# Performance work log

Measured on AMD Instinct MI355X. Metric: run time of the kernel, lower is better.

The kernel has to match this reference:

```python
import jax, jax.numpy as jnp
import numpy as np

N, E, F, H, G, C = 50000, 800000, 128, 64, 512, 10
RATIO = 0.5  # forward arg `ratio` baked as constant


def seg_mean(msgs, idx, n):
    s = jax.ops.segment_sum(msgs, idx, num_segments=n)
    cnt = jax.ops.segment_sum(jnp.ones(idx.shape[0], msgs.dtype), idx, num_segments=n)
    return s / jnp.maximum(cnt, 1.0)[:, None]


def sage(x, src, dst, Wl, bl, Wr, ew=None):
    # PyG SAGEConv: lin_l(mean_{j->i} msg_j) + lin_r(x_i); weighted variant scales messages
    m = x[src] if ew is None else x[src] * ew[:, None]
    agg = seg_mean(m, dst, x.shape[0])
    return agg @ Wl + bl + x @ Wr


def topk_mask(scores, seg, num_graphs, ratio):
    # per-graph (segment) top-k edge selection: keep ceil(ratio*edges_in_graph) highest scores
    e = scores.shape[0]
    counts = jax.ops.segment_sum(jnp.ones(e, jnp.float32), seg, num_segments=num_graphs)
    order = jnp.lexsort((-scores, seg))  # sort by segment, then score descending
    seg_sorted = seg[order]
    starts = jnp.concatenate([jnp.zeros(1, jnp.float32), jnp.cumsum(counts)[:-1]])
    rank = jnp.arange(e, dtype=jnp.float32) - starts[seg_sorted]
    k = jnp.ceil(ratio * counts)
    sel = (rank < k[seg_sorted]).astype(scores.dtype)
    return jnp.zeros(e, scores.dtype).at[order].set(sel)


def setup_inputs():
    key = jax.random.key(0)
    ks = jax.random.split(key, 16)
    w = lambda k, shape, fan: (jax.random.normal(k, shape, jnp.float32) / np.sqrt(fan))
    return {
        'x': jax.random.normal(ks[0], (N, F), jnp.float32),
        'edge_index': jax.random.randint(ks[1], (2, E), 0, N, jnp.int32),
        'batch': jnp.sort(jax.random.randint(ks[2], (N,), 0, G, jnp.int32)),
        'W1l': w(ks[3], (F, H), F), 'b1l': jnp.zeros(H, jnp.float32), 'W1r': w(ks[4], (F, H), F),
        'W2l': w(ks[5], (H, H), H), 'b2l': jnp.zeros(H, jnp.float32), 'W2r': w(ks[6], (H, H), H),
        'W3l': w(ks[7], (H, H), H), 'b3l': jnp.zeros(H, jnp.float32), 'W3r': w(ks[8], (H, H), H),
        'Wlin1': w(ks[9], (H, H), H), 'blin1': jnp.zeros(H, jnp.float32),
        'Wlin2': w(ks[10], (H, C), H), 'blin2': jnp.zeros(C, jnp.float32),
    }


def reference(x, edge_index, batch, W1l, b1l, W1r, W2l, b2l, W2r, W3l, b3l, W3r, Wlin1, blin1, Wlin2, blin2):
    src, dst = edge_index[0], edge_index[1]
    h = jax.nn.relu(sage(x, src, dst, W1l, b1l, W1r))
    edge_scores = jnp.sum(h[src] * h[dst], axis=-1)  # [E]
    seg = batch[src]  # graph id per edge (sections)
    sampled = topk_mask(edge_scores, seg, G, RATIO)
    ew = edge_scores * sampled
    h = jax.nn.relu(sage(h, src, dst, W2l, b2l, W2r, ew))
    h = jax.nn.relu(sage(h, src, dst, W3l, b3l, W3r, ew))
    pooled = seg_mean(h, batch, G)  # global_mean_pool
    z = jax.nn.relu(pooled @ Wlin1 + blin1)
    z = z @ Wlin2 + blin2  # dropout inactive in eval
    return jax.nn.log_softmax(z, axis=-1), sampled
```

## Files before the change

kernel.cpp:

```cpp
#include <hip/hip_runtime.h>
#include <hip/hip_bf16.h>
#include <math.h>

static constexpr int N = 50000;
static constexpr int E = 800000;
static constexpr int F = 128;
static constexpr int H = 64;
static constexpr int G = 512;
static constexpr int C = 10;
static constexpr int CAP = 256;
static constexpr int NFB = (E / 4 + 255) / 256;
static constexpr int GB1 = N / 16;
static constexpr int GB2 = (N + 31) / 32;
static constexpr int SB = E / 256;

static inline int cdiv(long a, int b) { return (int)((a + b - 1) / b); }

__device__ __forceinline__ float uinv_score(unsigned u) {
  return (u & 0x80000000u) ? __uint_as_float(u & 0x7fffffffu) : __uint_as_float(~u);
}

__device__ __forceinline__ int2 pack_slot(int s, int d, int g, int e) {
  unsigned a = (unsigned)s | ((unsigned)(d & 0x7FFF) << 17);
  unsigned b = ((unsigned)d >> 15) | ((unsigned)g << 2) | ((unsigned)e << 11);
  return make_int2((int)a, (int)b);
}
__device__ __forceinline__ int slot_src(int2 p) { return p.x & 0x1FFFF; }
__device__ __forceinline__ int slot_dst(int2 p) {
  return (int)(((unsigned)p.x >> 17) | (((unsigned)p.y & 3u) << 15));
}
__device__ __forceinline__ int slot_g(int2 p) { return (int)(((unsigned)p.y >> 2) & 0x1FFu); }
__device__ __forceinline__ int slot_eid(int2 p) { return (int)((unsigned)p.y >> 11); }

__global__ void k_deg_goff(const int* __restrict__ dst, const int* __restrict__ batch,
                           int* __restrict__ deg, int* __restrict__ goff,
                           unsigned short* __restrict__ rank16) {
  int tid = threadIdx.x;
  for (int i = blockIdx.x * 256 + tid; i < N; i += gridDim.x * 256) {
    int b = batch[i];
    if (i == 0) {
      for (int g = 0; g <= b; ++g) goff[g] = 0;
    } else {
      int p = batch[i - 1];
      for (int g = p + 1; g <= b; ++g) goff[g] = i;
    }
    if (i == N - 1) {
      for (int g = b + 1; g <= G; ++g) goff[g] = N;
    }
  }
  const int4* d4 = (const int4*)dst;
  for (int i = blockIdx.x * 256 + tid; i < E / 4; i += gridDim.x * 256) {
    int4 v = d4[i];
    ushort4 rk;
    rk.x = (unsigned short)atomicAdd(&deg[v.x], 1);
    rk.y = (unsigned short)atomicAdd(&deg[v.y], 1);
    rk.z = (unsigned short)atomicAdd(&deg[v.z], 1);
    rk.w = (unsigned short)atomicAdd(&deg[v.w], 1);
    *(ushort4*)(rank16 + (size_t)i * 4) = rk;
  }
}

__global__ void k_scan_a(const int* __restrict__ cnt, int* __restrict__ off,
                         int* __restrict__ bsum, int n) {
  __shared__ int wsum[16];
  int tid = threadIdx.x, lane = tid & 63, wv = tid >> 6;
  int idx = blockIdx.x * 4096 + tid * 4;
  int v0 = (idx + 0 < n) ? cnt[idx + 0] : 0;
  int v1 = (idx + 1 < n) ? cnt[idx + 1] : 0;
  int v2 = (idx + 2 < n) ? cnt[idx + 2] : 0;
  int v3 = (idx + 3 < n) ? cnt[idx + 3] : 0;
  int local = v0 + v1 + v2 + v3;
  int inc = local;
  for (int d = 1; d < 64; d <<= 1) {
    int t = __shfl_up(inc, d);
    if (lane >= d) inc += t;
  }
  if (lane == 63) wsum[wv] = inc;
  __syncthreads();
  if (tid < 16) {
    int t = wsum[tid];
    for (int d = 1; d < 16; d <<= 1) {
      int u = __shfl_up(t, d);
      if (tid >= d) t += u;
    }
    wsum[tid] = t;
  }
  __syncthreads();
  int woff = (wv > 0) ? wsum[wv - 1] : 0;
  int excl = woff + inc - local;
  if (idx + 0 < n) off[idx + 0] = excl;
  if (idx + 1 < n) off[idx + 1] = excl + v0;
  if (idx + 2 < n) off[idx + 2] = excl + v0 + v1;
  if (idx + 3 < n) off[idx + 3] = excl + v0 + v1 + v2;
  if (tid == 0) bsum[blockIdx.x] = wsum[15];
}

__global__ void k_scan_c(int* __restrict__ off, const int* __restrict__ bsum, int n, int nb) {
  __shared__ int spre[34];
  int tid = threadIdx.x;
  if (tid < 32) {
    int v = (tid < nb) ? bsum[tid] : 0;
    int inc = v;
    for (int d = 1; d < 32; d <<= 1) {
      int t = __shfl_up(inc, d);
      if (tid >= d) inc += t;
    }
    spre[tid] = inc - v;
  }
  __syncthreads();
  int i = blockIdx.x * 256 + tid;
  if (i < n) {
    off[i] = off[i] + spre[i >> 12];
  } else if (i == n) {
    off[n] = spre[nb];
  }
}

__global__ void k_fill_gemm(const int* __restrict__ src, const int* __restrict__ dst,
                            const unsigned short* __restrict__ rank16,
                            const int* __restrict__ batch, const int* __restrict__ off,
                            int2* __restrict__ csrp, int* __restrict__ einv,
                            const float* __restrict__ x, const float* __restrict__ Wl,
                            const float* __restrict__ Wr, const float* __restrict__ bl,
                            float* __restrict__ y, float* __restrict__ r) {
  __shared__ float sx[16][F];
  int lane = threadIdx.x, ty = threadIdx.y;
  int tid = ty * 64 + lane;
  int bq = blockIdx.x / 5, br = blockIdx.x - bq * 5;
  if (br == 0) {
    int i = bq * 256 + tid;
    if (i < E / 4) {
      int4 dv = ((const int4*)dst)[i];
      int4 sv = ((const int4*)src)[i];
      ushort4 rv = *(const ushort4*)(rank16 + (size_t)i * 4);
      int dd[4] = {dv.x, dv.y, dv.z, dv.w};
      int ss[4] = {sv.x, sv.y, sv.z, sv.w};
      int rr[4] = {rv.x, rv.y, rv.z, rv.w};
      int e0 = i * 4;
      int slots[4];
#pragma unroll
      for (int j = 0; j < 4; ++j) {
        int g = batch[ss[j]];
        int slot = off[dd[j]] + rr[j];
        csrp[slot] = pack_slot(ss[j], dd[j], g, e0 + j);
        slots[j] = slot;
      }
      *(int4*)(einv + e0) = make_int4(slots[0], slots[1], slots[2], slots[3]);
    }
    return;
  }
  int gid = bq * 4 + (br - 1);
  if (gid >= GB1) return;
  int row0 = gid * 16;
  const float4* gsrc = (const float4*)(x + (size_t)row0 * F);
  float4* sdst = (float4*)(&sx[0][0]);
#pragma unroll
  for (int i = tid; i < 16 * F / 4; i += 256) sdst[i] = gsrc[i];
  __syncthreads();
  float al[4], ar[4];
  float bias = bl[lane];
#pragma unroll
  for (int j = 0; j < 4; ++j) { al[j] = 0.f; ar[j] = bias; }
#pragma unroll 4
  for (int f = 0; f < F; ++f) {
    float wl = Wl[f * H + lane];
    float wr = Wr[f * H + lane];
#pragma unroll
    for (int j = 0; j < 4; ++j) {
      float xv = sx[ty * 4 + j][f];
      al[j] += xv * wl;
      ar[j] += xv * wr;
    }
  }
#pragma unroll
  for (int j = 0; j < 4; ++j) {
    int row = row0 + ty * 4 + j;
    y[(size_t)row * H + lane] = al[j];
    r[(size_t)row * H + lane] = ar[j];
  }
}

template <int K>
__global__ void k_gemm2h(const float* __restrict__ in, const float* __restrict__ Wl,
                         const float* __restrict__ Wr, const float* __restrict__ b,
                         __hip_bfloat16* __restrict__ y, float* __restrict__ r) {
  __shared__ float sx[16][K];
  int lane = threadIdx.x, ty = threadIdx.y;
  int tid = ty * 64 + lane;
  int row0 = blockIdx.x * 16;
  const float4* gsrc = (const float4*)(in + (size_t)row0 * K);
  float4* sdst = (float4*)(&sx[0][0]);
#pragma unroll
  for (int i = tid; i < 16 * K / 4; i += 256) sdst[i] = gsrc[i];
  __syncthreads();
  float al[4], ar[4];
  float bias = b[lane];
#pragma unroll
  for (int j = 0; j < 4; ++j) { al[j] = 0.f; ar[j] = bias; }
#pragma unroll 4
  for (int f = 0; f < K; ++f) {
    float wl = Wl[f * H + lane];
    float wr = Wr[f * H + lane];
#pragma unroll
    for (int j = 0; j < 4; ++j) {
      float xv = sx[ty * 4 + j][f];
      al[j] += xv * wl;
      ar[j] += xv * wr;
    }
  }
#pragma unroll
  for (int j = 0; j < 4; ++j) {
    int row = row0 + ty * 4 + j;
    y[(size_t)row * H + lane] = __float2bfloat16(al[j]);
    r[(size_t)row * H + lane] = ar[j];
  }
}

__global__ void k_agg1(const float* __restrict__ y, const float* __restrict__ r,
                       const int2* __restrict__ csrp, const int* __restrict__ off,
                       float* __restrict__ out) {
  int node = blockIdx.x * 8 + threadIdx.y;
  int lane = threadIdx.x;
  int q = lane >> 3, c = lane & 7;
  int s0 = off[node], s1 = off[node + 1];
  float4 a0 = make_float4(0.f, 0.f, 0.f, 0.f);
  float4 a1 = make_float4(0.f, 0.f, 0.f, 0.f);
  int i = s0 + q;
  for (; i + 8 < s1; i += 16) {
    int se0 = slot_src(csrp[i]);
    int se1 = slot_src(csrp[i + 8]);
    const float4* p0 = (const float4*)(y + (size_t)se0 * H);
    const float4* p1 = (const float4*)(y + (size_t)se1 * H);
    float4 u0 = p0[c], v0 = p0[c + 8];
    float4 u1 = p1[c], v1 = p1[c + 8];
    a0.x += u0.x + u1.x; a0.y += u0.y + u1.y; a0.z += u0.z + u1.z; a0.w += u0.w + u1.w;
    a1.x += v0.x + v1.x; a1.y += v0.y + v1.y; a1.z += v0.z + v1.z; a1.w += v0.w + v1.w;
  }
  for (; i < s1; i += 8) {
    int se = slot_src(csrp[i]);
    const float4* p = (const float4*)(y + (size_t)se * H);
    float4 u = p[c], v = p[c + 8];
    a0.x += u.x; a0.y += u.y; a0.z += u.z; a0.w += u.w;
    a1.x += v.x; a1.y += v.y; a1.z += v.z; a1.w += v.w;
  }
#pragma unroll
  for (int d = 8; d < 64; d <<= 1) {
    a0.x += __shfl_xor(a0.x, d); a0.y += __shfl_xor(a0.y, d);
    a0.z += __shfl_xor(a0.z, d); a0.w += __shfl_xor(a0.w, d);
    a1.x += __shfl_xor(a1.x, d); a1.y += __shfl_xor(a1.y, d);
    a1.z += __shfl_xor(a1.z, d); a1.w += __shfl_xor(a1.w, d);
  }
  if (q == 0) {
    float inv = 1.f / fmaxf((float)(s1 - s0), 1.f);
    const float4* rp = (const float4*)(r + (size_t)node * H);
    float4 r0 = rp[c], r1 = rp[c + 8];
    float4 o0, o1;
    o0.x = fmaxf(a0.x * inv + r0.x, 0.f); o0.y = fmaxf(a0.y * inv + r0.y, 0.f);
    o0.z = fmaxf(a0.z * inv + r0.z, 0.f); o0.w = fmaxf(a0.w * inv + r0.w, 0.f);
    o1.x = fmaxf(a1.x * inv + r1.x, 0.f); o1.y = fmaxf(a1.y * inv + r1.y, 0.f);
    o1.z = fmaxf(a1.z * inv + r1.z, 0.f); o1.w = fmaxf(a1.w * inv + r1.w, 0.f);
    float4* op = (float4*)(out + (size_t)node * H);
    op[c] = o0; op[c + 8] = o1;
  }
}

__global__ void k_agg_w(const __hip_bfloat16* __restrict__ y, const float* __restrict__ r,
                        const int2* __restrict__ csr2, const int* __restrict__ cnt2,
                        const int* __restrict__ off, float* __restrict__ out) {
  int node = blockIdx.x * 8 + threadIdx.y;
  int lane = threadIdx.x;
  int q = lane >> 3, c = lane & 7;
  int b0 = off[node], cn = cnt2[node];
  float a[8] = {0.f, 0.f, 0.f, 0.f, 0.f, 0.f, 0.f, 0.f};
  for (int j = q; j < cn; j += 8) {
    int2 sw = csr2[b0 + j];
    float w = __int_as_float(sw.y);
    uint4 pk = ((const uint4*)((const unsigned short*)y + (size_t)sw.x * H))[c];
    a[0] += w * __uint_as_float(pk.x << 16); a[1] += w * __uint_as_float(pk.x & 0xffff0000u);
    a[2] += w * __uint_as_float(pk.y << 16); a[3] += w * __uint_as_float(pk.y & 0xffff0000u);
    a[4] += w * __uint_as_float(pk.z << 16); a[5] += w * __uint_as_float(pk.z & 0xffff0000u);
    a[6] += w * __uint_as_float(pk.w << 16); a[7] += w * __uint_as_float(pk.w & 0xffff0000u);
  }
#pragma unroll
  for (int d = 8; d < 64; d <<= 1) {
#pragma unroll
    for (int j = 0; j < 8; ++j) a[j] += __shfl_xor(a[j], d);
  }
  if (q == 0) {
    int degn = off[node + 1] - off[node];
    float inv = 1.f / fmaxf((float)degn, 1.f);
    const float4* rp = (const float4*)(r + (size_t)node * H);
    float4 r0 = rp[2 * c], r1 = rp[2 * c + 1];
    float4 o0, o1;
    o0.x = fmaxf(a[0] * inv + r0.x, 0.f); o0.y = fmaxf(a[1] * inv + r0.y, 0.f);
    o0.z = fmaxf(a[2] * inv + r0.z, 0.f); o0.w = fmaxf(a[3] * inv + r0.w, 0.f);
    o1.x = fmaxf(a[4] * inv + r1.x, 0.f); o1.y = fmaxf(a[5] * inv + r1.y, 0.f);
    o1.z = fmaxf(a[6] * inv + r1.z, 0.f); o1.w = fmaxf(a[7] * inv + r1.w, 0.f);
    float4* op = (float4*)(out + (size_t)node * H);
    op[2 * c] = o0; op[2 * c + 1] = o1;
  }
}

__global__ void k_score_g2h(const float* __restrict__ h1, const int2* __restrict__ csrp,
                            unsigned* __restrict__ scoreu_csr,
                            unsigned short* __restrict__ seg_csr, int* __restrict__ hist,
                            const float* __restrict__ Wl, const float* __restrict__ Wr,
                            const float* __restrict__ bl,
                            __hip_bfloat16* __restrict__ y, float* __restrict__ r) {
  __shared__ float sx[32][H];
  int lane = threadIdx.x, ty = threadIdx.y;
  int q3 = blockIdx.x / 3, r3 = blockIdx.x - q3 * 3;
  if (r3 == 0 && q3 < GB2) {
    int tid = ty * 64 + lane;
    int row0 = q3 * 32;
    {
      int row = row0 + (tid >> 4);
      if (row < N)
        ((float4*)(&sx[0][0]))[tid] = ((const float4*)h1)[(size_t)row * (H / 4) + (tid & 15)];
    }
    __syncthreads();
    float al[4], ar[4];
    float bias = bl[lane];
#pragma unroll
    for (int j = 0; j < 4; ++j) { al[j] = 0.f; ar[j] = bias; }
#pragma unroll 4
    for (int f = 0; f < H; ++f) {
      float wl = Wl[f * H + lane];
      float wr = Wr[f * H + lane];
#pragma unroll
      for (int j = 0; j < 4; ++j) {
        float xv = sx[ty * 4 + j][f];
        al[j] += xv * wl;
        ar[j] += xv * wr;
      }
    }
#pragma unroll
    for (int j = 0; j < 4; ++j) {
      int row = row0 + ty * 4 + j;
      if (row < N) {
        y[(size_t)row * H + lane] = __float2bfloat16(al[j]);
        r[(size_t)row * H + lane] = ar[j];
      }
    }
  } else {
    int sid = blockIdx.x - (q3 + (r3 > 0 ? 1 : 0));
    int q = lane >> 4, c = lane & 15;
    int s = (sid * 8 + ty) * 32 + q * 8;
    int2 se[8];
#pragma unroll
    for (int j = 0; j < 8; ++j) se[j] = csrp[s + j];
    float4 xr[8], yr[8];
#pragma unroll
    for (int j = 0; j < 8; ++j)
      xr[j] = ((const float4*)(h1 + (size_t)slot_src(se[j]) * H))[c];
#pragma unroll
    for (int j = 0; j < 8; ++j)
      yr[j] = ((const float4*)(h1 + (size_t)slot_dst(se[j]) * H))[c];
    float p[8];
#pragma unroll
    for (int j = 0; j < 8; ++j)
      p[j] = yr[j].x * xr[j].x + yr[j].y * xr[j].y + yr[j].z * xr[j].z + yr[j].w * xr[j].w;
#pragma unroll
    for (int d = 1; d < 16; d <<= 1) {
#pragma unroll
      for (int j = 0; j < 8; ++j) p[j] += __shfl_xor(p[j], d);
    }
    if (c == 0) {
#pragma unroll
      for (int j = 0; j < 8; ++j) {
        int g = slot_g(se[j]);
        unsigned u = __float_as_uint(p[j]);
        u = (u & 0x80000000u) ? ~u : (u | 0x80000000u);
        scoreu_csr[s + j] = u;
        seg_csr[s + j] = (unsigned short)g;
        atomicAdd(&hist[g * 256 + (int)(u >> 24)], 1);
      }
    }
  }
}

__global__ void k_hist(const unsigned* __restrict__ scoreu, const unsigned short* __restrict__ seg,
                       const unsigned* __restrict__ prefix, int* __restrict__ hist, int pass) {
  int e = (blockIdx.x * 256 + threadIdx.x) * 4;
  if (e >= E) return;
  uint4 u4 = *(const uint4*)(scoreu + e);
  ushort4 s4 = *(const ushort4*)(seg + e);
  unsigned uu[4] = {u4.x, u4.y, u4.z, u4.w};
  int gg[4] = {(int)s4.x, (int)s4.y, (int)s4.z, (int)s4.w};
  int predshift = 32 - 8 * pass;
  int bshift = 24 - 8 * pass;
#pragma unroll
  for (int j = 0; j < 4; ++j) {
    unsigned u = uu[j];
    int g = gg[j];
    if ((u >> predshift) == (prefix[g] >> predshift))
      atomicAdd(&hist[g * 256 + (int)((u >> bshift) & 0xFFu)], 1);
  }
}

__global__ void k_scan(int* __restrict__ hist, unsigned* __restrict__ prefix,
                       int* __restrict__ krem, int pass) {
  int g = blockIdx.x;
  int lane = threadIdx.x;
  int4* row = (int4*)(hist + (size_t)g * 256);
  int4 v = row[lane];
  int vj[4] = {v.x, v.y, v.z, v.w};
  int s = v.x + v.y + v.z + v.w;
  int inc = s;
  for (int d = 1; d < 64; d <<= 1) {
    int t = __shfl_up(inc, d);
    if (lane >= d) inc += t;
  }
  int T = __shfl(inc, 63);
  int k = (pass == 0) ? ((T + 1) >> 1) : krem[g];
  int excl = inc - s;
  int pre[4] = {excl, excl + vj[0], excl + vj[0] + vj[1], excl + vj[0] + vj[1] + vj[2]};
  int bsel_l = -1, newk_l = 0;
  if (k > 0) {
    for (int j = 3; j >= 0; --j) {
      int suf = T - pre[j];
      if (suf >= k) { bsel_l = 4 * lane + j; newk_l = k - (suf - vj[j]); break; }
    }
  }
  unsigned long long mask = __ballot(bsel_l >= 0);
  int bsel = 255, newk = 0;
  if (k > 0 && mask) {
    int hi = 63 - __builtin_clzll(mask);
    bsel = __shfl(bsel_l, hi);
    newk = __shfl(newk_l, hi);
  }
  if (lane == 0) {
    unsigned base = (pass == 0) ? 0u : prefix[g];
    prefix[g] = base | ((unsigned)bsel << (24 - 8 * pass));
    krem[g] = newk;
  }
  row[lane] = make_int4(0, 0, 0, 0);
}

__global__ void k_select(const unsigned* __restrict__ scoreu_csr,
                         const unsigned short* __restrict__ seg_csr,
                         const unsigned* __restrict__ thresh,
                         int* __restrict__ eqcnt, int* __restrict__ eqlist,
                         unsigned char* __restrict__ sel_csr, float* __restrict__ ew_csr) {
  int s = (blockIdx.x * 256 + threadIdx.x) * 4;
  if (s >= E) return;
  uint4 u4 = *(const uint4*)(scoreu_csr + s);
  ushort4 g4 = *(const ushort4*)(seg_csr + s);
  unsigned uu[4] = {u4.x, u4.y, u4.z, u4.w};
  int gg[4] = {(int)g4.x, (int)g4.y, (int)g4.z, (int)g4.w};
  float ew[4];
  unsigned char sl[4];
#pragma unroll
  for (int j = 0; j < 4; ++j) {
    unsigned u = uu[j];
    int g = gg[j];
    unsigned t = thresh[g];
    unsigned um = u & 0xffffff00u;
    float sel = 0.f;
    if (um > t) sel = 1.f;
    else if (um == t) {
      int slot = atomicAdd(&eqcnt[g], 1);
      if (slot < CAP) eqlist[g * CAP + slot] = s + j;
    }
    sl[j] = (unsigned char)sel;
    ew[j] = uinv_score(u) * sel;
  }
  *(uchar4*)(sel_csr + s) = make_uchar4(sl[0], sl[1], sl[2], sl[3]);
  *(float4*)(ew_csr + s) = make_float4(ew[0], ew[1], ew[2], ew[3]);
}

__global__ void k_resolve(const int* __restrict__ krem, const int* __restrict__ eqcnt,
                          const int* __restrict__ eqlist, const int2* __restrict__ csrp,
                          const unsigned* __restrict__ scoreu_csr,
                          unsigned char* __restrict__ sel_csr, float* __restrict__ ew_csr) {
  int g = blockIdx.x * 256 + threadIdx.x;
  if (g >= G) return;
  int c = eqcnt[g]; if (c > CAP) c = CAP;
  int r = krem[g];  if (r > c) r = c;
  const int* lst = eqlist + g * CAP;
  unsigned last_u = 0u; int last_e = -1; bool first = true;
  for (int i = 0; i < r; ++i) {
    unsigned bu = 0u; int be = -1, bs = -1;
    for (int j = 0; j < c; ++j) {
      int slot = lst[j];
      unsigned u = scoreu_csr[slot];
      int eid = slot_eid(csrp[slot]);
      bool after = first || (u < last_u) || (u == last_u && eid > last_e);
      if (after && (bs < 0 || u > bu || (u == bu && eid < be))) { bu = u; be = eid; bs = slot; }
    }
    if (bs < 0) break;
    sel_csr[bs] = 1;
    ew_csr[bs] = uinv_score(bu);
    last_u = bu; last_e = be; first = false;
  }
}

__global__ void k_samp_comp(const unsigned char* __restrict__ sel,
                            const int2* __restrict__ csrp, const float* __restrict__ ewc,
                            const int* __restrict__ off, int2* __restrict__ csr2,
                            int* __restrict__ cnt2,
                            const int* __restrict__ einv, float* __restrict__ sampled) {
  int lane = threadIdx.x, ty = threadIdx.y;
  if (blockIdx.x < N / 8) {
    int node = blockIdx.x * 8 + ty;
    int s0 = off[node], s1 = off[node + 1];
    unsigned long long lt = ((unsigned long long)1 << lane) - 1;
    int cum = 0;
    for (int i0 = s0; i0 < s1; i0 += 64) {
      int i = i0 + lane;
      bool f = (i < s1) && sel[i];
      unsigned long long m = __ballot(f);
      if (f) {
        int rank = __popcll(m & lt);
        csr2[s0 + cum + rank] = make_int2(slot_src(csrp[i]), __float_as_int(ewc[i]));
      }
      cum += __popcll(m);
    }
    if (lane == 0) cnt2[node] = cum;
  } else {
    int tid = ty * 64 + lane;
    int e = ((blockIdx.x - N / 8) * 512 + tid) * 4;
    if (e >= E) return;
    int4 iv = *(const int4*)(einv + e);
    float4 o;
    o.x = (float)sel[iv.x];
    o.y = (float)sel[iv.y];
    o.z = (float)sel[iv.z];
    o.w = (float)sel[iv.w];
    *(float4*)(sampled + e) = o;
  }
}

__global__ void k_poolhead(const float* __restrict__ h3, const int* __restrict__ goff,
                           const float* __restrict__ W1, const float* __restrict__ b1,
                           const float* __restrict__ W2, const float* __restrict__ b2,
                           float* __restrict__ outp) {
  int g = blockIdx.x;
  int tid = threadIdx.x;
  int h = tid & 63, j = tid >> 6;
  int s0 = goff[g], s1 = goff[g + 1];
  float a = 0.f;
  for (int n = s0 + j; n < s1; n += 8) a += h3[(size_t)n * H + h];
  __shared__ float sp[8][H];
  __shared__ float p[H], z1[H], z2[C];
  __shared__ float lse;
  sp[j][h] = a;
  __syncthreads();
  if (j == 0) {
    float s = sp[0][h] + sp[1][h] + sp[2][h] + sp[3][h]
            + sp[4][h] + sp[5][h] + sp[6][h] + sp[7][h];
    float inv = 1.f / fmaxf((float)(s1 - s0), 1.f);
    p[h] = s * inv;
  }
  __syncthreads();
  if (j == 0) {
    float acc = b1[h];
#pragma unroll 8
    for (int f = 0; f < H; ++f) acc += p[f] * W1[f * H + h];
    z1[h] = fmaxf(acc, 0.f);
  }
  __syncthreads();
  if (tid < C) {
    float a2 = b2[tid];
#pragma unroll 8
    for (int f = 0; f < H; ++f) a2 += z1[f] * W2[f * C + tid];
    z2[tid] = a2;
  }
  __syncthreads();
  if (tid == 0) {
    float m = z2[0];
    for (int c = 1; c < C; ++c) m = fmaxf(m, z2[c]);
    float s = 0.f;
    for (int c = 0; c < C; ++c) s += expf(z2[c] - m);
    lse = m + logf(s);
  }
  __syncthreads();
  if (tid < C) outp[(size_t)g * C + tid] = z2[tid] - lse;
}

extern "C" void kernel_launch(void* const* d_in, const int* in_sizes, int n_in,
                              void* d_out, int out_size, void* d_ws, size_t ws_size,
                              hipStream_t stream) {
  const float* x     = (const float*)d_in[0];
  const int*   ei    = (const int*)d_in[1];
  const int*   batch = (const int*)d_in[2];
  const float* W1l   = (const float*)d_in[3];
  const float* b1l   = (const float*)d_in[4];
  const float* W1r   = (const float*)d_in[5];
  const float* W2l   = (const float*)d_in[6];
  const float* b2l   = (const float*)d_in[7];
  const float* W2r   = (const float*)d_in[8];
  const float* W3l   = (const float*)d_in[9];
  const float* b3l   = (const float*)d_in[10];
  const float* W3r   = (const float*)d_in[11];
  const float* Wlin1 = (const float*)d_in[12];
  const float* blin1 = (const float*)d_in[13];
  const float* Wlin2 = (const float*)d_in[14];
  const float* blin2 = (const float*)d_in[15];

  const int* srcv = ei;
  const int* dstv = ei + E;

  float* out_ls   = (float*)d_out;
  float* out_samp = out_ls + G * C;

  char* w = (char*)d_ws;
  auto carve = [&](size_t bytes) { void* p = (void*)w; w += (bytes + 255) & ~(size_t)255; return p; };
  char* zbase   = w;
  int*      deg     = (int*)carve((size_t)N * 4);
  int*      eqcnt   = (int*)carve((size_t)G * 4);
  int*      hist    = (int*)carve((size_t)G * 256 * 4);
  size_t    zbytes  = (size_t)(w - zbase);
  float*    h1      = (float*)carve((size_t)N * H * 4);
  float*    h2      = (float*)carve((size_t)N * H * 4);
  float*    h3      = (float*)carve((size_t)N * H * 4);
  float*    yb      = (float*)carve((size_t)N * H * 4);
  float*    rb      = (float*)carve((size_t)N * H * 4);
  __hip_bfloat16* ybh = (__hip_bfloat16*)carve((size_t)N * H * 2);
  unsigned* scoreu_csr = (unsigned*)carve((size_t)E * 4);
  unsigned short* seg_csr = (unsigned short*)carve((size_t)E * 2);
  float*    ew_csr     = (float*)carve((size_t)E * 4);
  unsigned char* sel_csr = (unsigned char*)carve((size_t)E);
  int2*     csrp    = (int2*)carve((size_t)E * 8);
  int*      einv    = (int*)carve((size_t)E * 4);
  unsigned short* rank16 = (unsigned short*)carve((size_t)E * 2);
  int*      off     = (int*)carve((size_t)(N + 1) * 4);
  int*      cnt2    = (int*)carve((size_t)N * 4);
  int*      goff    = (int*)carve((size_t)(G + 1) * 4);
  unsigned* prefix  = (unsigned*)carve((size_t)G * 4);
  int*      krem    = (int*)carve((size_t)G * 4);
  int*      eqlist  = (int*)carve((size_t)G * CAP * 4);
  int*      bsum    = (int*)carve((size_t)16 * 4);
  int2*     csr2    = (int2*)carve((size_t)E * 8);

  hipMemsetAsync(zbase, 0, zbytes, stream);

  k_deg_goff<<<256, 256, 0, stream>>>(dstv, batch, deg, goff, rank16);
  int nb = cdiv(N, 4096);
  k_scan_a<<<nb, 1024, 0, stream>>>(deg, off, bsum, N);
  k_scan_c<<<cdiv(N + 1, 256), 256, 0, stream>>>(off, bsum, N, nb);

  k_fill_gemm<<<5 * NFB, dim3(64, 4), 0, stream>>>(srcv, dstv, rank16, batch, off,
                                                   csrp, einv,
                                                   x, W1l, W1r, b1l, yb, rb);

  k_agg1<<<N / 8, dim3(64, 8), 0, stream>>>(yb, rb, csrp, off, h1);

  k_score_g2h<<<SB + GB2, dim3(64, 8), 0, stream>>>(h1, csrp, scoreu_csr, seg_csr, hist,
                                                    W2l, W2r, b2l, ybh, rb);
  k_scan<<<G, 64, 0, stream>>>(hist, prefix, krem, 0);
  for (int p = 1; p <= 2; ++p) {
    k_hist<<<cdiv(E / 4, 256), 256, 0, stream>>>(scoreu_csr, seg_csr, prefix, hist, p);
    k_scan<<<G, 64, 0, stream>>>(hist, prefix, krem, p);
  }
  k_select<<<cdiv(E / 4, 256), 256, 0, stream>>>(scoreu_csr, seg_csr, prefix,
                                                 eqcnt, eqlist, sel_csr, ew_csr);
  k_resolve<<<cdiv(G, 256), 256, 0, stream>>>(krem, eqcnt, eqlist, csrp, scoreu_csr,
                                              sel_csr, ew_csr);

  k_samp_comp<<<N / 8 + cdiv(E / 4, 512), dim3(64, 8), 0, stream>>>(
      sel_csr, csrp, ew_csr, off, csr2, cnt2, einv, out_samp);

  k_agg_w<<<N / 8, dim3(64, 8), 0, stream>>>(ybh, rb, csr2, cnt2, off, h2);

  k_gemm2h<H><<<N / 16, dim3(64, 4), 0, stream>>>(h2, W3l, W3r, b3l, ybh, rb);
  k_agg_w<<<N / 8, dim3(64, 8), 0, stream>>>(ybh, rb, csr2, cnt2, off, h3);

  k_poolhead<<<G, 512, 0, stream>>>(h3, goff, Wlin1, blin1, Wlin2, blin2, out_ls);
}
```

Measured before the change: 405.4 us.

## Fuse layer-2 aggregation with layer-3 GEMM and drop edge-weight buffer

Merges the weighted layer-2 aggregation with the layer-3 dual GEMM, so h2 stays in shared memory instead of being written to and reread from global memory, and one kernel launch goes away. The separate ew_csr array is removed: select and resolve now write only the selection flag, and the compaction kernel recomputes the weight from the score bits. The degree/graph-offset kernel also gets twice as many blocks. The fused GEMM runs per node with 64 threads reading W3 from global memory and no row tiling, so weight reuse may be lower than in the old 16-row GEMM. Separate ybh2/rb2 buffers are added so the kernel does not overwrite inputs that other blocks are still reading.

New measurement: 424.4 us. 4.7% more time.

```diff
diff --git a/kernel.cpp b/kernel.cpp
--- a/kernel.cpp
+++ b/kernel.cpp
@@ -180,42 +180,6 @@
   }
 }
 
-template <int K>
-__global__ void k_gemm2h(const float* __restrict__ in, const float* __restrict__ Wl,
-                         const float* __restrict__ Wr, const float* __restrict__ b,
-                         __hip_bfloat16* __restrict__ y, float* __restrict__ r) {
-  __shared__ float sx[16][K];
-  int lane = threadIdx.x, ty = threadIdx.y;
-  int tid = ty * 64 + lane;
-  int row0 = blockIdx.x * 16;
-  const float4* gsrc = (const float4*)(in + (size_t)row0 * K);
-  float4* sdst = (float4*)(&sx[0][0]);
-#pragma unroll
-  for (int i = tid; i < 16 * K / 4; i += 256) sdst[i] = gsrc[i];
-  __syncthreads();
-  float al[4], ar[4];
-  float bias = b[lane];
-#pragma unroll
-  for (int j = 0; j < 4; ++j) { al[j] = 0.f; ar[j] = bias; }
-#pragma unroll 4
-  for (int f = 0; f < K; ++f) {
-    float wl = Wl[f * H + lane];
-    float wr = Wr[f * H + lane];
-#pragma unroll
-    for (int j = 0; j < 4; ++j) {
-      float xv = sx[ty * 4 + j][f];
-      al[j] += xv * wl;
-      ar[j] += xv * wr;
-    }
-  }
-#pragma unroll
-  for (int j = 0; j < 4; ++j) {
-    int row = row0 + ty * 4 + j;
-    y[(size_t)row * H + lane] = __float2bfloat16(al[j]);
-    r[(size_t)row * H + lane] = ar[j];
-  }
-}
-
 __global__ void k_agg1(const float* __restrict__ y, const float* __restrict__ r,
                        const int2* __restrict__ csrp, const int* __restrict__ off,
                        float* __restrict__ out) {
@@ -264,6 +228,59 @@
   }
 }
 
+__global__ void k_agg_w_p3(const __hip_bfloat16* __restrict__ y, const float* __restrict__ r,
+                           const int2* __restrict__ csr2, const int* __restrict__ cnt2,
+                           const int* __restrict__ off, const unsigned* __restrict__ scoreu,
+                           const float* __restrict__ W3l, const float* __restrict__ W3r,
+                           const float* __restrict__ b3,
+                           __hip_bfloat16* __restrict__ ybh2, float* __restrict__ rb2) {
+  __shared__ float sh[8][H];
+  int node = blockIdx.x * 8 + threadIdx.y;
+  int lane = threadIdx.x;
+  int ty = threadIdx.y;
+  int q = lane >> 3, c = lane & 7;
+  int b0 = off[node], cn = cnt2[node];
+  float a[8] = {0.f, 0.f, 0.f, 0.f, 0.f, 0.f, 0.f, 0.f};
+  for (int j = q; j < cn; j += 8) {
+    int2 sw = csr2[b0 + j];
+    float w = __int_as_float(sw.y);
+    uint4 pk = ((const uint4*)((const unsigned short*)y + (size_t)sw.x * H))[c];
+    a[0] += w * __uint_as_float(pk.x << 16); a[1] += w * __uint_as_float(pk.x & 0xffff0000u);
+    a[2] += w * __uint_as_float(pk.y << 16); a[3] += w * __uint_as_float(pk.y & 0xffff0000u);
+    a[4] += w * __uint_as_float(pk.z << 16); a[5] += w * __uint_as_float(pk.z & 0xffff0000u);
+    a[6] += w * __uint_as_float(pk.w << 16); a[7] += w * __uint_as_float(pk.w & 0xffff0000u);
+  }
+#pragma unroll
+  for (int d = 8; d < 64; d <<= 1) {
+#pragma unroll
+    for (int j = 0; j < 8; ++j) a[j] += __shfl_xor(a[j], d);
+  }
+  if (q == 0) {
+    int degn = off[node + 1] - off[node];
+    float inv = 1.f / fmaxf((float)degn, 1.f);
+    const float4* rp = (const float4*)(r + (size_t)node * H);
+    float4 r0 = rp[2 * c], r1 = rp[2 * c + 1];
+    sh[ty][8 * c + 0] = fmaxf(a[0] * inv + r0.x, 0.f);
+    sh[ty][8 * c + 1] = fmaxf(a[1] * inv + r0.y, 0.f);
+    sh[ty][8 * c + 2] = fmaxf(a[2] * inv + r0.z, 0.f);
+    sh[ty][8 * c + 3] = fmaxf(a[3] * inv + r0.w, 0.f);
+    sh[ty][8 * c + 4] = fmaxf(a[4] * inv + r1.x, 0.f);
+    sh[ty][8 * c + 5] = fmaxf(a[5] * inv + r1.y, 0.f);
+    sh[ty][8 * c + 6] = fmaxf(a[6] * inv + r1.z, 0.f);
+    sh[ty][8 * c + 7] = fmaxf(a[7] * inv + r1.w, 0.f);
+  }
+  __syncthreads();
+  float al = 0.f, ar = b3[lane];
+#pragma unroll 4
+  for (int f = 0; f < H; ++f) {
+    float v = sh[ty][f];
+    al += v * W3l[f * H + lane];
+    ar += v * W3r[f * H + lane];
+  }
+  ybh2[(size_t)node * H + lane] = __float2bfloat16(al);
+  rb2[(size_t)node * H + lane] = ar;
+}
+
 __global__ void k_agg_w(const __hip_bfloat16* __restrict__ y, const float* __restrict__ r,
                         const int2* __restrict__ csr2, const int* __restrict__ cnt2,
                         const int* __restrict__ off, float* __restrict__ out) {
@@ -441,14 +458,13 @@
                          const unsigned short* __restrict__ seg_csr,
                          const unsigned* __restrict__ thresh,
                          int* __restrict__ eqcnt, int* __restrict__ eqlist,
-                         unsigned char* __restrict__ sel_csr, float* __restrict__ ew_csr) {
+                         unsigned char* __restrict__ sel_csr) {
   int s = (blockIdx.x * 256 + threadIdx.x) * 4;
   if (s >= E) return;
   uint4 u4 = *(const uint4*)(scoreu_csr + s);
   ushort4 g4 = *(const ushort4*)(seg_csr + s);
   unsigned uu[4] = {u4.x, u4.y, u4.z, u4.w};
   int gg[4] = {(int)g4.x, (int)g4.y, (int)g4.z, (int)g4.w};
-  float ew[4];
   unsigned char sl[4];
 #pragma unroll
   for (int j = 0; j < 4; ++j) {
@@ -456,23 +472,21 @@
     int g = gg[j];
     unsigned t = thresh[g];
     unsigned um = u & 0xffffff00u;
-    float sel = 0.f;
-    if (um > t) sel = 1.f;
+    unsigned char sel = 0;
+    if (um > t) sel = 1;
     else if (um == t) {
       int slot = atomicAdd(&eqcnt[g], 1);
       if (slot < CAP) eqlist[g * CAP + slot] = s + j;
     }
-    sl[j] = (unsigned char)sel;
-    ew[j] = uinv_score(u) * sel;
+    sl[j] = sel;
   }
   *(uchar4*)(sel_csr + s) = make_uchar4(sl[0], sl[1], sl[2], sl[3]);
-  *(float4*)(ew_csr + s) = make_float4(ew[0], ew[1], ew[2], ew[3]);
 }
 
 __global__ void k_resolve(const int* __restrict__ krem, const int* __restrict__ eqcnt,
                           const int* __restrict__ eqlist, const int2* __restrict__ csrp,
                           const unsigned* __restrict__ scoreu_csr,
-                          unsigned char* __restrict__ sel_csr, float* __restrict__ ew_csr) {
+                          unsigned char* __restrict__ sel_csr) {
   int g = blockIdx.x * 256 + threadIdx.x;
   if (g >= G) return;
   int c = eqcnt[g]; if (c > CAP) c = CAP;
@@ -490,13 +504,13 @@
     }
     if (bs < 0) break;
     sel_csr[bs] = 1;
-    ew_csr[bs] = uinv_score(bu);
     last_u = bu; last_e = be; first = false;
   }
 }
 
 __global__ void k_samp_comp(const unsigned char* __restrict__ sel,
-                            const int2* __restrict__ csrp, const float* __restrict__ ewc,
+                            const int2* __restrict__ csrp,
+                            const unsigned* __restrict__ scoreu,
                             const int* __restrict__ off, int2* __restrict__ csr2,
                             int* __restrict__ cnt2,
                             const int* __restrict__ einv, float* __restrict__ sampled) {
@@ -512,7 +526,8 @@
       unsigned long long m = __ballot(f);
       if (f) {
         int rank = __popcll(m & lt);
-        csr2[s0 + cum + rank] = make_int2(slot_src(csrp[i]), __float_as_int(ewc[i]));
+        float w = uinv_score(scoreu[i]);
+        csr2[s0 + cum + rank] = make_int2(slot_src(csrp[i]), __float_as_int(w));
       }
       cum += __popcll(m);
     }
@@ -612,14 +627,14 @@
   int*      hist    = (int*)carve((size_t)G * 256 * 4);
   size_t    zbytes  = (size_t)(w - zbase);
   float*    h1      = (float*)carve((size_t)N * H * 4);
-  float*    h2      = (float*)carve((size_t)N * H * 4);
   float*    h3      = (float*)carve((size_t)N * H * 4);
   float*    yb      = (float*)carve((size_t)N * H * 4);
   float*    rb      = (float*)carve((size_t)N * H * 4);
-  __hip_bfloat16* ybh = (__hip_bfloat16*)carve((size_t)N * H * 2);
+  float*    rb2     = (float*)carve((size_t)N * H * 4);
+  __hip_bfloat16* ybh  = (__hip_bfloat16*)carve((size_t)N * H * 2);
+  __hip_bfloat16* ybh2 = (__hip_bfloat16*)carve((size_t)N * H * 2);
   unsigned* scoreu_csr = (unsigned*)carve((size_t)E * 4);
   unsigned short* seg_csr = (unsigned short*)carve((size_t)E * 2);
-  float*    ew_csr     = (float*)carve((size_t)E * 4);
   unsigned char* sel_csr = (unsigned char*)carve((size_t)E);
   int2*     csrp    = (int2*)carve((size_t)E * 8);
   int*      einv    = (int*)carve((size_t)E * 4);
@@ -635,7 +650,7 @@
 
   hipMemsetAsync(zbase, 0, zbytes, stream);
 
-  k_deg_goff<<<256, 256, 0, stream>>>(dstv, batch, deg, goff, rank16);
+  k_deg_goff<<<512, 256, 0, stream>>>(dstv, batch, deg, goff, rank16);
   int nb = cdiv(N, 4096);
   k_scan_a<<<nb, 1024, 0, stream>>>(deg, off, bsum, N);
   k_scan_c<<<cdiv(N + 1, 256), 256, 0, stream>>>(off, bsum, N, nb);
@@ -654,17 +669,17 @@
     k_scan<<<G, 64, 0, stream>>>(hist, prefix, krem, p);
   }
   k_select<<<cdiv(E / 4, 256), 256, 0, stream>>>(scoreu_csr, seg_csr, prefix,
-                                                 eqcnt, eqlist, sel_csr, ew_csr);
+                                                 eqcnt, eqlist, sel_csr);
   k_resolve<<<cdiv(G, 256), 256, 0, stream>>>(krem, eqcnt, eqlist, csrp, scoreu_csr,
-                                              sel_csr, ew_csr);
+                                              sel_csr);
 
   k_samp_comp<<<N / 8 + cdiv(E / 4, 512), dim3(64, 8), 0, stream>>>(
-      sel_csr, csrp, ew_csr, off, csr2, cnt2, einv, out_samp);
-
-  k_agg_w<<<N / 8, dim3(64, 8), 0, stream>>>(ybh, rb, csr2, cnt2, off, h2);
-
-  k_gemm2h<H><<<N / 16, dim3(64, 4), 0, stream>>>(h2, W3l, W3r, b3l, ybh, rb);
-  k_agg_w<<<N / 8, dim3(64, 8), 0, stream>>>(ybh, rb, csr2, cnt2, off, h3);
+      sel_csr, csrp, scoreu_csr, off, csr2, cnt2, einv, out_samp);
+
+  k_agg_w_p3<<<N / 8, dim3(64, 8), 0, stream>>>(ybh, rb, csr2, cnt2, off, scoreu_csr,
+                                                W3l, W3r, b3l, ybh2, rb2);
+
+  k_agg_w<<<N / 8, dim3(64, 8), 0, stream>>>(ybh2, rb2, csr2, cnt2, off, h3);
 
   k_poolhead<<<G, 512, 0, stream>>>(h3, goff, Wlin1, blin1, Wlin2, blin2, out_ls);
 }
```
